# Kernel optimization log

Measured on AMD Instinct MI355X. Metric: run time of the kernel, lower is better.

The kernel has to match this reference:

```python
import jax, jax.numpy as jnp
import numpy as np

N, E, D, C, T, G, L = 50000, 640000, 128, 128, 10, 512, 3


def setup_inputs() -> dict:
    key = jax.random.key(0)
    ks = jax.random.split(key, 8)
    x = jax.random.normal(ks[0], (N, D), dtype=jnp.float32)
    edge_index = jax.random.randint(ks[1], (2, E), 0, N, dtype=jnp.int64)
    batch = jnp.sort(jax.random.randint(ks[2], (N,), 0, G, dtype=jnp.int64))
    s = 0.05
    W1 = jax.random.normal(ks[3], (D, C), dtype=jnp.float32) * s
    b1 = jnp.zeros((C,), dtype=jnp.float32)
    Ws = jax.random.normal(ks[4], (L, C, C), dtype=jnp.float32) * s
    bs = jnp.zeros((L, C), dtype=jnp.float32)
    Wlin = jax.random.normal(ks[5], (C, T), dtype=jnp.float32) * s
    blin = jnp.zeros((T,), dtype=jnp.float32)
    return {"x": x, "edge_index": edge_index, "batch": batch,
            "W1": W1, "b1": b1, "Ws": Ws, "bs": bs,
            "Wlin": Wlin, "blin": blin}


def _gcn_norm(edge_index, n_nodes):
    # PyG GCNConv: add self-loops, symmetric normalization D^-1/2 A_hat D^-1/2
    loop = jnp.arange(n_nodes, dtype=edge_index.dtype)
    src = jnp.concatenate([edge_index[0], loop])
    dst = jnp.concatenate([edge_index[1], loop])
    deg = jax.ops.segment_sum(jnp.ones_like(dst, dtype=jnp.float32), dst,
                              num_segments=n_nodes)
    dinv = jax.lax.rsqrt(jnp.maximum(deg, 1.0))
    norm = dinv[src] * dinv[dst]  # [E + N]
    return src, dst, norm


def _gcn_conv(h, W, b, src, dst, norm, n_nodes):
    h = h @ W                              # [N, C] linear transform (no bias)
    msg = norm[:, None] * h[src]           # gather + scale, [E+N, C]
    out = jax.ops.segment_sum(msg, dst, num_segments=n_nodes)  # scatter-add
    return out + b


def reference(x, edge_index, batch, W1, b1, Ws, bs, Wlin, blin):
    n_nodes = x.shape[0]
    src, dst, norm = _gcn_norm(edge_index, n_nodes)
    h = jax.nn.relu(_gcn_conv(x, W1, b1, src, dst, norm, n_nodes))
    n_layers = Ws.shape[0]
    for i in range(n_layers):
        h = _gcn_conv(h, Ws[i], bs[i], src, dst, norm, n_nodes)
        if i != n_layers - 1:
            h = jax.nn.relu(h)
    # global_mean_pool over graph ids
    sums = jax.ops.segment_sum(h, batch, num_segments=G)        # [G, C]
    cnts = jax.ops.segment_sum(jnp.ones((n_nodes,), h.dtype), batch,
                               num_segments=G)
    pooled = sums / jnp.maximum(cnts, 1.0)[:, None]
    # dropout p=0 is identity
    return pooled @ Wlin + blin                                  # [G, T]
```

## Files before the change

kernel.cpp:

```cpp
#include <hip/hip_runtime.h>
#include <hip/hip_fp16.h>


__global__ void k_count(const int* __restrict__ dstv, int E, int* __restrict__ cnt) {
    int e = blockIdx.x * blockDim.x + threadIdx.x;
    if (e < E) atomicAdd(&cnt[dstv[e]], 1);
}

__global__ void k_scan1(const int* __restrict__ cnt, int N,
                        int* __restrict__ rowptr, int* __restrict__ bsums,
                        float* __restrict__ dinv) {
    __shared__ int sh[256];
    const int t = threadIdx.x;
    const int i = blockIdx.x * 256 + t;
    const int v = (i < N) ? cnt[i] : 0;
    const int pv = (v + 3) & ~3;
    if (i < N) dinv[i] = 1.0f / sqrtf((float)(v + 1));
    sh[t] = pv;
    __syncthreads();
    for (int off = 1; off < 256; off <<= 1) {
        int add = (t >= off) ? sh[t - off] : 0;
        __syncthreads();
        sh[t] += add;
        __syncthreads();
    }
    if (i < N) rowptr[i] = sh[t] - pv;
    if (t == 255) bsums[blockIdx.x] = sh[255];
}

__global__ void k_scan2(int* __restrict__ bsums, int nb) {
    __shared__ int sh[256];
    const int t = threadIdx.x;
    const int v = (t < nb) ? bsums[t] : 0;
    sh[t] = v;
    __syncthreads();
    for (int off = 1; off < 256; off <<= 1) {
        int add = (t >= off) ? sh[t - off] : 0;
        __syncthreads();
        sh[t] += add;
        __syncthreads();
    }
    if (t < nb) bsums[t] = sh[t] - v;
}

__global__ void k_scan3(int* __restrict__ rowptr, const int* __restrict__ bsums,
                        int* __restrict__ cnt, int N) {
    const int i = blockIdx.x * blockDim.x + threadIdx.x;
    if (i < N) {
        rowptr[i] += bsums[i >> 8];
        if (i == N - 1) rowptr[N] = rowptr[i] + ((cnt[i] + 3) & ~3);
        cnt[i] = 0;
    }
}

__global__ void k_fill(const int* __restrict__ srcv, const int* __restrict__ dstv,
                       const int* __restrict__ rowptr, int* __restrict__ cur,
                       const float* __restrict__ dinv,
                       float2* __restrict__ csr_pack, int E) {
    int e = blockIdx.x * blockDim.x + threadIdx.x;
    if (e < E) {
        const int d = dstv[e];
        const int s = srcv[e];
        const int slot = atomicAdd(&cur[d], 1);
        float2 rec;
        rec.x = __int_as_float(s);
        rec.y = dinv[s] * dinv[d];
        csr_pack[rowptr[d] + slot] = rec;
    }
}

__global__ void k_bounds(const int* __restrict__ batch, int N, int G,
                         int* __restrict__ start) {
    const int g = blockIdx.x * blockDim.x + threadIdx.x;
    if (g > G) return;
    int lo = 0, hi = N;
    while (lo < hi) {
        const int mid = (lo + hi) >> 1;
        if (batch[mid] < g) lo = mid + 1; else hi = mid;
    }
    start[g] = lo;
}

__global__ void k_combine(const float* __restrict__ W4, const float* __restrict__ Wlin,
                          const float* __restrict__ b4, const float* __restrict__ blin,
                          float* __restrict__ Wc, float* __restrict__ bc, int T) {
    const int idx = blockIdx.x * blockDim.x + threadIdx.x;
    if (idx < 128 * T) {
        const int k = idx / T, t = idx % T;
        float acc = 0.f;
        #pragma unroll 8
        for (int j = 0; j < 128; ++j)
            acc = fmaf(W4[k * 128 + j], Wlin[j * T + t], acc);
        Wc[idx] = acc;
    }
    if (idx < T) {
        float acc = blin[idx];
        #pragma unroll 8
        for (int j = 0; j < 128; ++j)
            acc = fmaf(b4[j], Wlin[j * T + idx], acc);
        bc[idx] = acc;
    }
}

__device__ __forceinline__ void fma4(float4& acc, float s, const float4& w) {
    acc.x = fmaf(s, w.x, acc.x);
    acc.y = fmaf(s, w.y, acc.y);
    acc.z = fmaf(s, w.z, acc.z);
    acc.w = fmaf(s, w.w, acc.w);
}

__device__ __forceinline__ float4 ld_h4(const __half* p) {
    const float2 raw = *(const float2*)p;
    const __half2* hp = (const __half2*)&raw;
    const float2 f01 = __half22float2(hp[0]);
    const float2 f23 = __half22float2(hp[1]);
    return make_float4(f01.x, f01.y, f23.x, f23.y);
}

__device__ __forceinline__ void st_h4(__half* p, float4 v) {
    float2 raw;
    ((__half2*)&raw)[0] = __floats2half2_rn(v.x, v.y);
    ((__half2*)&raw)[1] = __floats2half2_rn(v.z, v.w);
    *(float2*)p = raw;
}

__global__ void k_cvt(const float* __restrict__ in, __half* __restrict__ out, int n4) {
    int i = blockIdx.x * blockDim.x + threadIdx.x;
    if (i < n4) {
        const float4 v = ((const float4*)in)[i];
        st_h4(out + 4 * i, v);
    }
}

__device__ __forceinline__ void gather_pair2(
    int n0, int n1, int v0, int v1,
    const __half* __restrict__ Hin,
    const int* __restrict__ rowptr, const float2* __restrict__ pk,
    const float* __restrict__ dinv, int lane, int dummy,
    float4& r0, float4& r1)
{
    const int nc0 = v0 ? n0 : 0;
    const int nc1 = v1 ? n1 : 0;
    const float dn0 = v0 ? dinv[nc0] : 0.f;
    const float dn1 = v1 ? dinv[nc1] : 0.f;
    int c0 = rowptr[nc0];
    int c1 = rowptr[nc1];
    const int e0 = v0 ? rowptr[nc0 + 1] : c0;
    const int e1 = v1 ? rowptr[nc1 + 1] : c1;

    const float4 s0v = ld_h4(Hin + (size_t)nc0 * 128 + 4 * lane);
    const float4 s1v = ld_h4(Hin + (size_t)nc1 * 128 + 4 * lane);
    const float sw0 = dn0 * dn0, sw1 = dn1 * dn1;
    float4 p0 = make_float4(s0v.x * sw0, s0v.y * sw0, s0v.z * sw0, s0v.w * sw0);
    float4 q0 = make_float4(s1v.x * sw1, s1v.y * sw1, s1v.z * sw1, s1v.w * sw1);
    float4 p1 = make_float4(0.f, 0.f, 0.f, 0.f);
    float4 q1 = make_float4(0.f, 0.f, 0.f, 0.f);

    while (c0 < e0 || c1 < e1) {
        const int a0 = (c0 < e0) ? c0 : dummy;
        const int a1 = (c1 < e1) ? c1 : dummy;
        const float2 ra0 = pk[a0];
        const float2 ra1 = pk[a0 + 1];
        const float2 ra2 = pk[a0 + 2];
        const float2 ra3 = pk[a0 + 3];
        const float2 rb0 = pk[a1];
        const float2 rb1 = pk[a1 + 1];
        const float2 rb2 = pk[a1 + 2];
        const float2 rb3 = pk[a1 + 3];
        const float4 va0 = ld_h4(Hin + (size_t)__float_as_int(ra0.x) * 128 + 4 * lane);
        const float4 va1 = ld_h4(Hin + (size_t)__float_as_int(ra1.x) * 128 + 4 * lane);
        const float4 va2 = ld_h4(Hin + (size_t)__float_as_int(ra2.x) * 128 + 4 * lane);
        const float4 va3 = ld_h4(Hin + (size_t)__float_as_int(ra3.x) * 128 + 4 * lane);
        const float4 vb0 = ld_h4(Hin + (size_t)__float_as_int(rb0.x) * 128 + 4 * lane);
        const float4 vb1 = ld_h4(Hin + (size_t)__float_as_int(rb1.x) * 128 + 4 * lane);
        const float4 vb2 = ld_h4(Hin + (size_t)__float_as_int(rb2.x) * 128 + 4 * lane);
        const float4 vb3 = ld_h4(Hin + (size_t)__float_as_int(rb3.x) * 128 + 4 * lane);
        fma4(p0, ra0.y, va0); fma4(p1, ra1.y, va1);
        fma4(p0, ra2.y, va2); fma4(p1, ra3.y, va3);
        fma4(q0, rb0.y, vb0); fma4(q1, rb1.y, vb1);
        fma4(q0, rb2.y, vb2); fma4(q1, rb3.y, vb3);
        c0 += 4; c1 += 4;
    }
    p0.x += p1.x; p0.y += p1.y; p0.z += p1.z; p0.w += p1.w;
    q0.x += q1.x; q0.y += q1.y; q0.z += q1.z; q0.w += q1.w;
    r0 = p0;
    r1 = q0;
}

__global__ __launch_bounds__(512, 6) void k_layer(
    const __half* __restrict__ Hin, const float* __restrict__ W,
    const float* __restrict__ bias,
    const int* __restrict__ rowptr, const float2* __restrict__ csr_pack,
    const float* __restrict__ dinv, int dummy,
    __half* __restrict__ Hout, int N)
{
    __shared__ float Wl[64 * 128];
    __shared__ float hl[32 * 128];
    const int tid = threadIdx.x;
    for (int i = tid; i < 2048; i += 512)
        ((float4*)Wl)[i] = ((const float4*)W)[i];

    const int lane = tid & 31;
    const int grp  = tid >> 5;
    const int rowBase = blockIdx.x << 5;

    const int n0 = rowBase + grp;
    const int n1 = rowBase + grp + 16;
    const int v0 = n0 < N, v1 = n1 < N;
    float4 g0, g1;
    gather_pair2(n0, n1, v0, v1, Hin, rowptr, csr_pack, dinv, lane, dummy, g0, g1);
    if (v0) *(float4*)(hl + grp * 128 + 4 * lane) = g0;
    if (v1) *(float4*)(hl + (grp + 16) * 128 + 4 * lane) = g1;
    __syncthreads();

    float4 a0 = make_float4(0.f, 0.f, 0.f, 0.f);
    float4 a1 = make_float4(0.f, 0.f, 0.f, 0.f);
    #pragma unroll 4
    for (int kq = 0; kq < 16; ++kq) {
        const float4 h0 = *(const float4*)(hl + grp * 128 + 4 * kq);
        const float4 h1 = *(const float4*)(hl + (grp + 16) * 128 + 4 * kq);
        const float4* wp = ((const float4*)Wl) + (4 * kq) * 32 + lane;
        const float4 w0 = wp[0];
        const float4 w1 = wp[32];
        const float4 w2 = wp[64];
        const float4 w3 = wp[96];
        fma4(a0, h0.x, w0); fma4(a0, h0.y, w1); fma4(a0, h0.z, w2); fma4(a0, h0.w, w3);
        fma4(a1, h1.x, w0); fma4(a1, h1.y, w1); fma4(a1, h1.z, w2); fma4(a1, h1.w, w3);
    }
    __syncthreads();
    for (int i = tid; i < 2048; i += 512)
        ((float4*)Wl)[i] = ((const float4*)(W + 64 * 128))[i];
    __syncthreads();
    #pragma unroll 4
    for (int kq = 0; kq < 16; ++kq) {
        const float4 h0 = *(const float4*)(hl + grp * 128 + 64 + 4 * kq);
        const float4 h1 = *(const float4*)(hl + (grp + 16) * 128 + 64 + 4 * kq);
        const float4* wp = ((const float4*)Wl) + (4 * kq) * 32 + lane;
        const float4 w0 = wp[0];
        const float4 w1 = wp[32];
        const float4 w2 = wp[64];
        const float4 w3 = wp[96];
        fma4(a0, h0.x, w0); fma4(a0, h0.y, w1); fma4(a0, h0.z, w2); fma4(a0, h0.w, w3);
        fma4(a1, h1.x, w0); fma4(a1, h1.y, w1); fma4(a1, h1.z, w2); fma4(a1, h1.w, w3);
    }

    const float4 bv = ((const float4*)bias)[lane];
    a0.x += bv.x; a0.y += bv.y; a0.z += bv.z; a0.w += bv.w;
    a1.x += bv.x; a1.y += bv.y; a1.z += bv.z; a1.w += bv.w;
    a0.x = fmaxf(a0.x, 0.f); a0.y = fmaxf(a0.y, 0.f);
    a0.z = fmaxf(a0.z, 0.f); a0.w = fmaxf(a0.w, 0.f);
    a1.x = fmaxf(a1.x, 0.f); a1.y = fmaxf(a1.y, 0.f);
    a1.z = fmaxf(a1.z, 0.f); a1.w = fmaxf(a1.w, 0.f);
    if (v0) st_h4(Hout + (size_t)n0 * 128 + 4 * lane, a0);
    if (v1) st_h4(Hout + (size_t)n1 * 128 + 4 * lane, a1);
}

__global__ __launch_bounds__(256) void k_gather4(
    const int* __restrict__ rowptr, const float2* __restrict__ csr_pack,
    const float* __restrict__ dinv, const __half* __restrict__ Hin,
    __half* __restrict__ outb, int dummy, int N)
{
    const int t = blockIdx.x * blockDim.x + threadIdx.x;
    const int lane = t & 31;
    const int g = t >> 5;
    const int n0 = 2 * g, n1 = 2 * g + 1;
    if (n0 >= N) return;
    float4 r0, r1;
    gather_pair2(n0, n1, 1, n1 < N, Hin, rowptr, csr_pack, dinv, lane, dummy, r0, r1);
    st_h4(outb + (size_t)n0 * 128 + 4 * lane, r0);
    if (n1 < N) st_h4(outb + (size_t)n1 * 128 + 4 * lane, r1);
}

__global__ void k_pool_seg(const __half* __restrict__ h, const int* __restrict__ start,
                           float* __restrict__ pooled)
{
    __shared__ float4 sh[8][32];
    const int g = blockIdx.x;
    const int t = threadIdx.x;
    const int lane = t & 31, grp = t >> 5;
    const int s0 = start[g], s1 = start[g + 1];

    float4 acc = make_float4(0.f, 0.f, 0.f, 0.f);
    for (int r = s0 + grp; r < s1; r += 8) {
        const float4 v = ld_h4(h + (size_t)r * 128 + 4 * lane);
        acc.x += v.x; acc.y += v.y; acc.z += v.z; acc.w += v.w;
    }
    sh[grp][lane] = acc;
    __syncthreads();
    if (grp == 0) {
        float4 a = sh[0][lane];
        #pragma unroll
        for (int k = 1; k < 8; ++k) {
            a.x += sh[k][lane].x; a.y += sh[k][lane].y;
            a.z += sh[k][lane].z; a.w += sh[k][lane].w;
        }
        const float inv = 1.0f / fmaxf((float)(s1 - s0), 1.0f);
        a.x *= inv; a.y *= inv; a.z *= inv; a.w *= inv;
        *(float4*)(pooled + (size_t)g * 128 + 4 * lane) = a;
    }
}

__global__ void k_final(const float* __restrict__ pooled, const float* __restrict__ Wc,
                        const float* __restrict__ bc, float* __restrict__ out, int T)
{
    __shared__ float hv[128];
    const int g = blockIdx.x;
    const int c = threadIdx.x;
    hv[c] = pooled[(size_t)g * 128 + c];
    __syncthreads();
    if (c < T) {
        float acc = bc[c];
        #pragma unroll
        for (int k = 0; k < 128; ++k)
            acc = fmaf(hv[k], Wc[k * T + c], acc);
        out[g * T + c] = acc;
    }
}

extern "C" void kernel_launch(void* const* d_in, const int* in_sizes, int n_in,
                              void* d_out, int out_size, void* d_ws, size_t ws_size,
                              hipStream_t stream)
{
    const float* x     = (const float*)d_in[0];
    const int*   ei    = (const int*)d_in[1];
    const int*   batch = (const int*)d_in[2];
    const float* W1    = (const float*)d_in[3];
    const float* b1    = (const float*)d_in[4];
    const float* Ws    = (const float*)d_in[5];
    const float* bs    = (const float*)d_in[6];
    const float* Wlin  = (const float*)d_in[7];
    const float* blin  = (const float*)d_in[8];
    float* out = (float*)d_out;

    const int N = in_sizes[0] / 128;
    const int E = in_sizes[1] / 2;
    const int T = in_sizes[8];
    const int G = out_size / T;

    const int packCap = E + 3 * N + 4;
    const int dummy   = E + 3 * N;

    float*  ws = (float*)d_ws;
    int*    cnt      = (int*)ws;
    float*  Wc       = ws + 24000;
    float*  bc       = ws + 24000 + 128 * 10;
    int*    rowptr   = (int*)(ws + 50000);
    int*    bsums    = (int*)(ws + 100016);
    int*    start    = (int*)(ws + 100272);
    float2* csr_pack = (float2*)(ws + 100800);
    float*  dinv     = ws + 1680816;
    __half* x16      = (__half*)(ws + 1730816);
    __half* bufA16   = (__half*)(ws + 4930816);
    __half* bufB16   = (__half*)(ws + 8130816);
    float*  pooled   = ws + 11330816;

    const int* srcs = ei;
    const int* dsts = ei + E;
    const float* W4 = Ws + 2 * 16384;
    const float* b4 = bs + 2 * 128;

    hipMemsetAsync(cnt, 0, (size_t)N * sizeof(int), stream);
    hipMemsetAsync(csr_pack, 0, (size_t)packCap * sizeof(float2), stream);

    const int nb = (N + 255) / 256;
    k_count <<<(E + 255) / 256, 256, 0, stream>>>(dsts, E, cnt);
    k_scan1 <<<nb, 256, 0, stream>>>(cnt, N, rowptr, bsums, dinv);
    k_scan2 <<<1, 256, 0, stream>>>(bsums, nb);
    k_scan3 <<<nb, 256, 0, stream>>>(rowptr, bsums, cnt, N);
    k_fill  <<<(E + 255) / 256, 256, 0, stream>>>(srcs, dsts, rowptr, cnt, dinv, csr_pack, E);
    k_bounds<<<(G + 256) / 256, 256, 0, stream>>>(batch, N, G, start);
    k_combine<<<(128 * T + 255) / 256, 256, 0, stream>>>(W4, Wlin, b4, blin, Wc, bc, T);
    k_cvt   <<<(N * 32 + 255) / 256, 256, 0, stream>>>(x, x16, N * 32);

    const int layerBlocks = (N + 31) / 32;

    k_layer<<<layerBlocks, 512, 0, stream>>>(x16,    W1,         b1,       rowptr, csr_pack, dinv, dummy, bufA16, N);
    k_layer<<<layerBlocks, 512, 0, stream>>>(bufA16, Ws,         bs,       rowptr, csr_pack, dinv, dummy, bufB16, N);
    k_layer<<<layerBlocks, 512, 0, stream>>>(bufB16, Ws + 16384, bs + 128, rowptr, csr_pack, dinv, dummy, bufA16, N);
    const int g4blocks = (((N + 1) / 2) * 32 + 255) / 256;
    k_gather4<<<g4blocks, 256, 0, stream>>>(rowptr, csr_pack, dinv, bufA16, bufB16, dummy, N);

    k_pool_seg<<<G, 256, 0, stream>>>(bufB16, start, pooled);
    k_final   <<<G, 128, 0, stream>>>(pooled, Wc, bc, out, T);
}
```

Before: 288.9 us.

## Fuse final gather with pooling and readout, merge setup kernels

Folds the three small setup kernels (fp16 convert, weight/Wlin combine, batch bounds) into one launch with block-range dispatch. Replaces the last-layer gather, segment pooling and final linear with a single per-graph kernel that gathers each node's neighbours and reduces them directly into the pooled vector. This drops the intermediate fp16 write/read of the last aggregation and cuts several launches. It also converts halves to float inline during the FMAs and unrolls the matmul FMAs, and moves workspace offsets. The trade-off is that the tail now runs only G=512 blocks, so parallelism depends on per-graph node counts and may load-imbalance.

```diff
diff --git a/kernel.cpp b/kernel.cpp
--- a/kernel.cpp
+++ b/kernel.cpp
@@ -69,54 +69,6 @@
     }
 }
 
-__global__ void k_bounds(const int* __restrict__ batch, int N, int G,
-                         int* __restrict__ start) {
-    const int g = blockIdx.x * blockDim.x + threadIdx.x;
-    if (g > G) return;
-    int lo = 0, hi = N;
-    while (lo < hi) {
-        const int mid = (lo + hi) >> 1;
-        if (batch[mid] < g) lo = mid + 1; else hi = mid;
-    }
-    start[g] = lo;
-}
-
-__global__ void k_combine(const float* __restrict__ W4, const float* __restrict__ Wlin,
-                          const float* __restrict__ b4, const float* __restrict__ blin,
-                          float* __restrict__ Wc, float* __restrict__ bc, int T) {
-    const int idx = blockIdx.x * blockDim.x + threadIdx.x;
-    if (idx < 128 * T) {
-        const int k = idx / T, t = idx % T;
-        float acc = 0.f;
-        #pragma unroll 8
-        for (int j = 0; j < 128; ++j)
-            acc = fmaf(W4[k * 128 + j], Wlin[j * T + t], acc);
-        Wc[idx] = acc;
-    }
-    if (idx < T) {
-        float acc = blin[idx];
-        #pragma unroll 8
-        for (int j = 0; j < 128; ++j)
-            acc = fmaf(b4[j], Wlin[j * T + idx], acc);
-        bc[idx] = acc;
-    }
-}
-
-__device__ __forceinline__ void fma4(float4& acc, float s, const float4& w) {
-    acc.x = fmaf(s, w.x, acc.x);
-    acc.y = fmaf(s, w.y, acc.y);
-    acc.z = fmaf(s, w.z, acc.z);
-    acc.w = fmaf(s, w.w, acc.w);
-}
-
-__device__ __forceinline__ float4 ld_h4(const __half* p) {
-    const float2 raw = *(const float2*)p;
-    const __half2* hp = (const __half2*)&raw;
-    const float2 f01 = __half22float2(hp[0]);
-    const float2 f23 = __half22float2(hp[1]);
-    return make_float4(f01.x, f01.y, f23.x, f23.y);
-}
-
 __device__ __forceinline__ void st_h4(__half* p, float4 v) {
     float2 raw;
     ((__half2*)&raw)[0] = __floats2half2_rn(v.x, v.y);
@@ -124,12 +76,56 @@
     *(float2*)p = raw;
 }
 
-__global__ void k_cvt(const float* __restrict__ in, __half* __restrict__ out, int n4) {
-    int i = blockIdx.x * blockDim.x + threadIdx.x;
-    if (i < n4) {
-        const float4 v = ((const float4*)in)[i];
-        st_h4(out + 4 * i, v);
-    }
+__global__ void k_setup(const float* __restrict__ x, __half* __restrict__ x16, int n4,
+                        const float* __restrict__ W4, const float* __restrict__ Wlin,
+                        const float* __restrict__ b4, const float* __restrict__ blin,
+                        float* __restrict__ Wc, float* __restrict__ bc, int T,
+                        const int* __restrict__ batch, int N, int G,
+                        int* __restrict__ start, int cvtB, int cmbB)
+{
+    const int b = blockIdx.x;
+    const int t = threadIdx.x;
+    if (b < cvtB) {
+        const int i = b * 256 + t;
+        if (i < n4) {
+            const float4 v = ((const float4*)x)[i];
+            st_h4(x16 + 4 * i, v);
+        }
+    } else if (b < cvtB + cmbB) {
+        const int idx = (b - cvtB) * 256 + t;
+        if (idx < 128 * T) {
+            const int k = idx / T, tt = idx % T;
+            float acc = 0.f;
+            #pragma unroll 8
+            for (int j = 0; j < 128; ++j)
+                acc = fmaf(W4[k * 128 + j], Wlin[j * T + tt], acc);
+            Wc[idx] = acc;
+        }
+        if (idx < T) {
+            float acc = blin[idx];
+            #pragma unroll 8
+            for (int j = 0; j < 128; ++j)
+                acc = fmaf(b4[j], Wlin[j * T + idx], acc);
+            bc[idx] = acc;
+        }
+    } else {
+        const int g = (b - cvtB - cmbB) * 256 + t;
+        if (g > G) return;
+        int lo = 0, hi = N;
+        while (lo < hi) {
+            const int mid = (lo + hi) >> 1;
+            if (batch[mid] < g) lo = mid + 1; else hi = mid;
+        }
+        start[g] = lo;
+    }
+}
+
+__device__ __forceinline__ void fma4mix(float4& acc, float s, uint2 raw) {
+    const __half* h = (const __half*)&raw;
+    acc.x = fmaf(s, __half2float(h[0]), acc.x);
+    acc.y = fmaf(s, __half2float(h[1]), acc.y);
+    acc.z = fmaf(s, __half2float(h[2]), acc.z);
+    acc.w = fmaf(s, __half2float(h[3]), acc.w);
 }
 
 __device__ __forceinline__ void gather_pair2(
@@ -148,13 +144,14 @@
     const int e0 = v0 ? rowptr[nc0 + 1] : c0;
     const int e1 = v1 ? rowptr[nc1 + 1] : c1;
 
-    const float4 s0v = ld_h4(Hin + (size_t)nc0 * 128 + 4 * lane);
-    const float4 s1v = ld_h4(Hin + (size_t)nc1 * 128 + 4 * lane);
-    const float sw0 = dn0 * dn0, sw1 = dn1 * dn1;
-    float4 p0 = make_float4(s0v.x * sw0, s0v.y * sw0, s0v.z * sw0, s0v.w * sw0);
-    float4 q0 = make_float4(s1v.x * sw1, s1v.y * sw1, s1v.z * sw1, s1v.w * sw1);
+    const uint2 s0v = *(const uint2*)(Hin + (size_t)nc0 * 128 + 4 * lane);
+    const uint2 s1v = *(const uint2*)(Hin + (size_t)nc1 * 128 + 4 * lane);
+    float4 p0 = make_float4(0.f, 0.f, 0.f, 0.f);
+    float4 q0 = make_float4(0.f, 0.f, 0.f, 0.f);
     float4 p1 = make_float4(0.f, 0.f, 0.f, 0.f);
     float4 q1 = make_float4(0.f, 0.f, 0.f, 0.f);
+    fma4mix(p0, dn0 * dn0, s0v);
+    fma4mix(q0, dn1 * dn1, s1v);
 
     while (c0 < e0 || c1 < e1) {
         const int a0 = (c0 < e0) ? c0 : dummy;
@@ -167,18 +164,18 @@
         const float2 rb1 = pk[a1 + 1];
         const float2 rb2 = pk[a1 + 2];
         const float2 rb3 = pk[a1 + 3];
-        const float4 va0 = ld_h4(Hin + (size_t)__float_as_int(ra0.x) * 128 + 4 * lane);
-        const float4 va1 = ld_h4(Hin + (size_t)__float_as_int(ra1.x) * 128 + 4 * lane);
-        const float4 va2 = ld_h4(Hin + (size_t)__float_as_int(ra2.x) * 128 + 4 * lane);
-        const float4 va3 = ld_h4(Hin + (size_t)__float_as_int(ra3.x) * 128 + 4 * lane);
-        const float4 vb0 = ld_h4(Hin + (size_t)__float_as_int(rb0.x) * 128 + 4 * lane);
-        const float4 vb1 = ld_h4(Hin + (size_t)__float_as_int(rb1.x) * 128 + 4 * lane);
-        const float4 vb2 = ld_h4(Hin + (size_t)__float_as_int(rb2.x) * 128 + 4 * lane);
-        const float4 vb3 = ld_h4(Hin + (size_t)__float_as_int(rb3.x) * 128 + 4 * lane);
-        fma4(p0, ra0.y, va0); fma4(p1, ra1.y, va1);
-        fma4(p0, ra2.y, va2); fma4(p1, ra3.y, va3);
-        fma4(q0, rb0.y, vb0); fma4(q1, rb1.y, vb1);
-        fma4(q0, rb2.y, vb2); fma4(q1, rb3.y, vb3);
+        const uint2 va0 = *(const uint2*)(Hin + (size_t)__float_as_int(ra0.x) * 128 + 4 * lane);
+        const uint2 va1 = *(const uint2*)(Hin + (size_t)__float_as_int(ra1.x) * 128 + 4 * lane);
+        const uint2 va2 = *(const uint2*)(Hin + (size_t)__float_as_int(ra2.x) * 128 + 4 * lane);
+        const uint2 va3 = *(const uint2*)(Hin + (size_t)__float_as_int(ra3.x) * 128 + 4 * lane);
+        const uint2 vb0 = *(const uint2*)(Hin + (size_t)__float_as_int(rb0.x) * 128 + 4 * lane);
+        const uint2 vb1 = *(const uint2*)(Hin + (size_t)__float_as_int(rb1.x) * 128 + 4 * lane);
+        const uint2 vb2 = *(const uint2*)(Hin + (size_t)__float_as_int(rb2.x) * 128 + 4 * lane);
+        const uint2 vb3 = *(const uint2*)(Hin + (size_t)__float_as_int(rb3.x) * 128 + 4 * lane);
+        fma4mix(p0, ra0.y, va0); fma4mix(p1, ra1.y, va1);
+        fma4mix(p0, ra2.y, va2); fma4mix(p1, ra3.y, va3);
+        fma4mix(q0, rb0.y, vb0); fma4mix(q1, rb1.y, vb1);
+        fma4mix(q0, rb2.y, vb2); fma4mix(q1, rb3.y, vb3);
         c0 += 4; c1 += 4;
     }
     p0.x += p1.x; p0.y += p1.y; p0.z += p1.z; p0.w += p1.w;
@@ -224,8 +221,22 @@
         const float4 w1 = wp[32];
         const float4 w2 = wp[64];
         const float4 w3 = wp[96];
-        fma4(a0, h0.x, w0); fma4(a0, h0.y, w1); fma4(a0, h0.z, w2); fma4(a0, h0.w, w3);
-        fma4(a1, h1.x, w0); fma4(a1, h1.y, w1); fma4(a1, h1.z, w2); fma4(a1, h1.w, w3);
+        a0.x = fmaf(h0.x, w0.x, a0.x); a0.y = fmaf(h0.x, w0.y, a0.y);
+        a0.z = fmaf(h0.x, w0.z, a0.z); a0.w = fmaf(h0.x, w0.w, a0.w);
+        a0.x = fmaf(h0.y, w1.x, a0.x); a0.y = fmaf(h0.y, w1.y, a0.y);
+        a0.z = fmaf(h0.y, w1.z, a0.z); a0.w = fmaf(h0.y, w1.w, a0.w);
+        a0.x = fmaf(h0.z, w2.x, a0.x); a0.y = fmaf(h0.z, w2.y, a0.y);
+        a0.z = fmaf(h0.z, w2.z, a0.z); a0.w = fmaf(h0.z, w2.w, a0.w);
+        a0.x = fmaf(h0.w, w3.x, a0.x); a0.y = fmaf(h0.w, w3.y, a0.y);
+        a0.z = fmaf(h0.w, w3.z, a0.z); a0.w = fmaf(h0.w, w3.w, a0.w);
+        a1.x = fmaf(h1.x, w0.x, a1.x); a1.y = fmaf(h1.x, w0.y, a1.y);
+        a1.z = fmaf(h1.x, w0.z, a1.z); a1.w = fmaf(h1.x, w0.w, a1.w);
+        a1.x = fmaf(h1.y, w1.x, a1.x); a1.y = fmaf(h1.y, w1.y, a1.y);
+        a1.z = fmaf(h1.y, w1.z, a1.z); a1.w = fmaf(h1.y, w1.w, a1.w);
+        a1.x = fmaf(h1.z, w2.x, a1.x); a1.y = fmaf(h1.z, w2.y, a1.y);
+        a1.z = fmaf(h1.z, w2.z, a1.z); a1.w = fmaf(h1.z, w2.w, a1.w);
+        a1.x = fmaf(h1.w, w3.x, a1.x); a1.y = fmaf(h1.w, w3.y, a1.y);
+        a1.z = fmaf(h1.w, w3.z, a1.z); a1.w = fmaf(h1.w, w3.w, a1.w);
     }
     __syncthreads();
     for (int i = tid; i < 2048; i += 512)
@@ -240,8 +251,22 @@
         const float4 w1 = wp[32];
         const float4 w2 = wp[64];
         const float4 w3 = wp[96];
-        fma4(a0, h0.x, w0); fma4(a0, h0.y, w1); fma4(a0, h0.z, w2); fma4(a0, h0.w, w3);
-        fma4(a1, h1.x, w0); fma4(a1, h1.y, w1); fma4(a1, h1.z, w2); fma4(a1, h1.w, w3);
+        a0.x = fmaf(h0.x, w0.x, a0.x); a0.y = fmaf(h0.x, w0.y, a0.y);
+        a0.z = fmaf(h0.x, w0.z, a0.z); a0.w = fmaf(h0.x, w0.w, a0.w);
+        a0.x = fmaf(h0.y, w1.x, a0.x); a0.y = fmaf(h0.y, w1.y, a0.y);
+        a0.z = fmaf(h0.y, w1.z, a0.z); a0.w = fmaf(h0.y, w1.w, a0.w);
+        a0.x = fmaf(h0.z, w2.x, a0.x); a0.y = fmaf(h0.z, w2.y, a0.y);
+        a0.z = fmaf(h0.z, w2.z, a0.z); a0.w = fmaf(h0.z, w2.w, a0.w);
+        a0.x = fmaf(h0.w, w3.x, a0.x); a0.y = fmaf(h0.w, w3.y, a0.y);
+        a0.z = fmaf(h0.w, w3.z, a0.z); a0.w = fmaf(h0.w, w3.w, a0.w);
+        a1.x = fmaf(h1.x, w0.x, a1.x); a1.y = fmaf(h1.x, w0.y, a1.y);
+        a1.z = fmaf(h1.x, w0.z, a1.z); a1.w = fmaf(h1.x, w0.w, a1.w);
+        a1.x = fmaf(h1.y, w1.x, a1.x); a1.y = fmaf(h1.y, w1.y, a1.y);
+        a1.z = fmaf(h1.y, w1.z, a1.z); a1.w = fmaf(h1.y, w1.w, a1.w);
+        a1.x = fmaf(h1.z, w2.x, a1.x); a1.y = fmaf(h1.z, w2.y, a1.y);
+        a1.z = fmaf(h1.z, w2.z, a1.z); a1.w = fmaf(h1.z, w2.w, a1.w);
+        a1.x = fmaf(h1.w, w3.x, a1.x); a1.y = fmaf(h1.w, w3.y, a1.y);
+        a1.z = fmaf(h1.w, w3.z, a1.z); a1.w = fmaf(h1.w, w3.w, a1.w);
     }
 
     const float4 bv = ((const float4*)bias)[lane];
@@ -255,65 +280,47 @@
     if (v1) st_h4(Hout + (size_t)n1 * 128 + 4 * lane, a1);
 }
 
-__global__ __launch_bounds__(256) void k_gather4(
+__global__ __launch_bounds__(512) void k_tail(
     const int* __restrict__ rowptr, const float2* __restrict__ csr_pack,
     const float* __restrict__ dinv, const __half* __restrict__ Hin,
-    __half* __restrict__ outb, int dummy, int N)
-{
-    const int t = blockIdx.x * blockDim.x + threadIdx.x;
-    const int lane = t & 31;
-    const int g = t >> 5;
-    const int n0 = 2 * g, n1 = 2 * g + 1;
-    if (n0 >= N) return;
-    float4 r0, r1;
-    gather_pair2(n0, n1, 1, n1 < N, Hin, rowptr, csr_pack, dinv, lane, dummy, r0, r1);
-    st_h4(outb + (size_t)n0 * 128 + 4 * lane, r0);
-    if (n1 < N) st_h4(outb + (size_t)n1 * 128 + 4 * lane, r1);
-}
-
-__global__ void k_pool_seg(const __half* __restrict__ h, const int* __restrict__ start,
-                           float* __restrict__ pooled)
-{
-    __shared__ float4 sh[8][32];
+    const int* __restrict__ startv,
+    const float* __restrict__ Wc, const float* __restrict__ bc,
+    float* __restrict__ out, int dummy, int T)
+{
+    __shared__ float red[16 * 128];
     const int g = blockIdx.x;
-    const int t = threadIdx.x;
-    const int lane = t & 31, grp = t >> 5;
-    const int s0 = start[g], s1 = start[g + 1];
+    const int tid = threadIdx.x;
+    const int lane = tid & 31;
+    const int grp  = tid >> 5;
+    const int s0 = startv[g], s1 = startv[g + 1];
 
     float4 acc = make_float4(0.f, 0.f, 0.f, 0.f);
-    for (int r = s0 + grp; r < s1; r += 8) {
-        const float4 v = ld_h4(h + (size_t)r * 128 + 4 * lane);
-        acc.x += v.x; acc.y += v.y; acc.z += v.z; acc.w += v.w;
-    }
-    sh[grp][lane] = acc;
-    __syncthreads();
-    if (grp == 0) {
-        float4 a = sh[0][lane];
+    for (int r = s0 + grp; r < s1; r += 32) {
+        const int n1 = r + 16;
+        float4 r0, r1;
+        gather_pair2(r, n1, 1, n1 < s1, Hin, rowptr, csr_pack, dinv, lane, dummy, r0, r1);
+        acc.x += r0.x + r1.x; acc.y += r0.y + r1.y;
+        acc.z += r0.z + r1.z; acc.w += r0.w + r1.w;
+    }
+    *(float4*)(red + grp * 128 + 4 * lane) = acc;
+    __syncthreads();
+
+    if (tid < 128) {
+        float s = 0.f;
         #pragma unroll
-        for (int k = 1; k < 8; ++k) {
-            a.x += sh[k][lane].x; a.y += sh[k][lane].y;
-            a.z += sh[k][lane].z; a.w += sh[k][lane].w;
-        }
+        for (int k = 0; k < 16; ++k)
+            s += red[k * 128 + tid];
         const float inv = 1.0f / fmaxf((float)(s1 - s0), 1.0f);
-        a.x *= inv; a.y *= inv; a.z *= inv; a.w *= inv;
-        *(float4*)(pooled + (size_t)g * 128 + 4 * lane) = a;
-    }
-}
-
-__global__ void k_final(const float* __restrict__ pooled, const float* __restrict__ Wc,
-                        const float* __restrict__ bc, float* __restrict__ out, int T)
-{
-    __shared__ float hv[128];
-    const int g = blockIdx.x;
-    const int c = threadIdx.x;
-    hv[c] = pooled[(size_t)g * 128 + c];
-    __syncthreads();
-    if (c < T) {
-        float acc = bc[c];
-        #pragma unroll
+        red[tid] = s * inv;
+    }
+    __syncthreads();
+
+    if (tid < T) {
+        float o = bc[tid];
+        #pragma unroll 8
         for (int k = 0; k < 128; ++k)
-            acc = fmaf(hv[k], Wc[k * T + c], acc);
-        out[g * T + c] = acc;
+            o = fmaf(red[k], Wc[k * T + tid], o);
+        out[g * T + tid] = o;
     }
 }
 
@@ -342,17 +349,16 @@
 
     float*  ws = (float*)d_ws;
     int*    cnt      = (int*)ws;
-    float*  Wc       = ws + 24000;
-    float*  bc       = ws + 24000 + 128 * 10;
     int*    rowptr   = (int*)(ws + 50000);
     int*    bsums    = (int*)(ws + 100016);
     int*    start    = (int*)(ws + 100272);
     float2* csr_pack = (float2*)(ws + 100800);
-    float*  dinv     = ws + 1680816;
-    __half* x16      = (__half*)(ws + 1730816);
-    __half* bufA16   = (__half*)(ws + 4930816);
-    __half* bufB16   = (__half*)(ws + 8130816);
-    float*  pooled   = ws + 11330816;
+    float*  dinv     = ws + 1780816;
+    __half* x16      = (__half*)(ws + 1830816);
+    __half* bufA16   = (__half*)(ws + 5030816);
+    __half* bufB16   = (__half*)(ws + 8230816);
+    float*  Wc       = ws + 11430816;
+    float*  bc       = ws + 11430816 + 128 * 10;
 
     const int* srcs = ei;
     const int* dsts = ei + E;
@@ -368,18 +374,19 @@
     k_scan2 <<<1, 256, 0, stream>>>(bsums, nb);
     k_scan3 <<<nb, 256, 0, stream>>>(rowptr, bsums, cnt, N);
     k_fill  <<<(E + 255) / 256, 256, 0, stream>>>(srcs, dsts, rowptr, cnt, dinv, csr_pack, E);
-    k_bounds<<<(G + 256) / 256, 256, 0, stream>>>(batch, N, G, start);
-    k_combine<<<(128 * T + 255) / 256, 256, 0, stream>>>(W4, Wlin, b4, blin, Wc, bc, T);
-    k_cvt   <<<(N * 32 + 255) / 256, 256, 0, stream>>>(x, x16, N * 32);
+
+    const int cvtB = (N * 32 + 255) / 256;
+    const int cmbB = (128 * T + 255) / 256;
+    const int bndB = (G + 256) / 256;
+    k_setup<<<cvtB + cmbB + bndB, 256, 0, stream>>>(
+        x, x16, N * 32, W4, Wlin, b4, blin, Wc, bc, T,
+        batch, N, G, start, cvtB, cmbB);
 
     const int layerBlocks = (N + 31) / 32;
 
     k_layer<<<layerBlocks, 512, 0, stream>>>(x16,    W1,         b1,       rowptr, csr_pack, dinv, dummy, bufA16, N);
     k_layer<<<layerBlocks, 512, 0, stream>>>(bufA16, Ws,         bs,       rowptr, csr_pack, dinv, dummy, bufB16, N);
     k_layer<<<layerBlocks, 512, 0, stream>>>(bufB16, Ws + 16384, bs + 128, rowptr, csr_pack, dinv, dummy, bufA16, N);
-    const int g4blocks = (((N + 1) / 2) * 32 + 255) / 256;
-    k_gather4<<<g4blocks, 256, 0, stream>>>(rowptr, csr_pack, dinv, bufA16, bufB16, dummy, N);
-
-    k_pool_seg<<<G, 256, 0, stream>>>(bufB16, start, pooled);
-    k_final   <<<G, 128, 0, stream>>>(pooled, Wc, bc, out, T);
-}
+
+    k_tail<<<G, 512, 0, stream>>>(rowptr, csr_pack, dinv, bufA16, start, Wc, bc, out, dummy, T);
+}
```

Result: faster. 279.1 us (-3.4%).
